# Optimization experiments

Hardware: AMD Instinct MI355X
Metric: run time of the kernel (lower is better)

The kernel has to match this reference:

```python
import jax, jax.numpy as jnp
import numpy as np

B, S, IN_F, OUT_F, GROUP = 2, 1024, 4096, 4096, 128
N_GROUPS = IN_F // GROUP  # 32


def setup_inputs() -> dict:
    key = jax.random.key(0)
    k1, k2, k3, k4 = jax.random.split(key, 4)
    x = jax.random.normal(k1, (B, S, IN_F), dtype=jnp.float32)
    # int4-range weights stored in int8, symmetric quant in [-7, 7]
    w_q = jax.random.randint(k2, (OUT_F, N_GROUPS, GROUP), -7, 8, dtype=jnp.int8)
    # per-(group, out_feature) scales, positive
    s_w = jax.random.uniform(k3, (N_GROUPS, OUT_F), dtype=jnp.float32,
                             minval=1e-3, maxval=2e-2)
    bias = jax.random.normal(k4, (OUT_F,), dtype=jnp.float32)
    return {"x": x, "w_q": w_q, "s_w": s_w, "bias": bias}


def reference(x, w_q, s_w, bias):
    # Faithful to QuantLinearW4Grouped.forward:
    #   y_g = einsum('ngk,ogk->ngo', x_f, w_f); y = (y_g * s_w[None]).sum(1) + bias
    # Expressed as a single fused einsum (identical math, no (n,g,o) intermediate).
    prefix = x.shape[:-1]
    orig_dtype = x.dtype
    xg = x.reshape(-1, N_GROUPS, GROUP).astype(jnp.float32)  # (n, g, k)
    w_f = w_q.astype(jnp.float32)                            # (o, g, k)
    y = jnp.einsum('ngk,ogk,go->no', xg, w_f, s_w)           # (n, o)
    y = y + bias.astype(y.dtype)
    return y.reshape(*prefix, OUT_F).astype(orig_dtype)
```

## Files before the change

### kernel.cpp

```cpp
#include <hip/hip_runtime.h>
#include <hip/hip_bf16.h>
#include <stdint.h>

#define M_TOK 2048
#define N_OUT 4096
#define K_IN  4096
#define GROUPSZ 128
#define NGRP  32

typedef signed char i8;
typedef int    intx4  __attribute__((ext_vector_type(4)));
typedef float  floatx4 __attribute__((ext_vector_type(4)));

#define XQ_BLOCKS (M_TOK)
#define WQ_BLOCKS (N_OUT * K_IN / 16 / 256)

__global__ __launch_bounds__(256) void quant_kernel(
    const float* __restrict__ x, const int* __restrict__ wq,
    i8* __restrict__ xq, i8* __restrict__ wq8, float* __restrict__ sx) {
  __shared__ float red[4];
  int b = blockIdx.x;
  int tid = threadIdx.x;
  if (b < XQ_BLOCKS) {
    const float* xr = x + (size_t)b * K_IN;
    int e0 = tid * 16;
    float4 v0 = *(const float4*)(xr + e0);
    float4 v1 = *(const float4*)(xr + e0 + 4);
    float4 v2 = *(const float4*)(xr + e0 + 8);
    float4 v3 = *(const float4*)(xr + e0 + 12);
    float m = fabsf(v0.x);
    m = fmaxf(m, fabsf(v0.y)); m = fmaxf(m, fabsf(v0.z)); m = fmaxf(m, fabsf(v0.w));
    m = fmaxf(m, fabsf(v1.x)); m = fmaxf(m, fabsf(v1.y)); m = fmaxf(m, fabsf(v1.z)); m = fmaxf(m, fabsf(v1.w));
    m = fmaxf(m, fabsf(v2.x)); m = fmaxf(m, fabsf(v2.y)); m = fmaxf(m, fabsf(v2.z)); m = fmaxf(m, fabsf(v2.w));
    m = fmaxf(m, fabsf(v3.x)); m = fmaxf(m, fabsf(v3.y)); m = fmaxf(m, fabsf(v3.z)); m = fmaxf(m, fabsf(v3.w));
#pragma unroll
    for (int off = 32; off > 0; off >>= 1)
      m = fmaxf(m, __shfl_xor(m, off, 64));
    int lane = tid & 63, wv = tid >> 6;
    if (lane == 0) red[wv] = m;
    __syncthreads();
    m = fmaxf(fmaxf(red[0], red[1]), fmaxf(red[2], red[3]));
    float inv = (m > 0.f) ? 127.f / m : 0.f;
    union { i8 q[16]; int4 v; } u;
    u.q[0]  = (i8)(int)rintf(v0.x * inv); u.q[1]  = (i8)(int)rintf(v0.y * inv);
    u.q[2]  = (i8)(int)rintf(v0.z * inv); u.q[3]  = (i8)(int)rintf(v0.w * inv);
    u.q[4]  = (i8)(int)rintf(v1.x * inv); u.q[5]  = (i8)(int)rintf(v1.y * inv);
    u.q[6]  = (i8)(int)rintf(v1.z * inv); u.q[7]  = (i8)(int)rintf(v1.w * inv);
    u.q[8]  = (i8)(int)rintf(v2.x * inv); u.q[9]  = (i8)(int)rintf(v2.y * inv);
    u.q[10] = (i8)(int)rintf(v2.z * inv); u.q[11] = (i8)(int)rintf(v2.w * inv);
    u.q[12] = (i8)(int)rintf(v3.x * inv); u.q[13] = (i8)(int)rintf(v3.y * inv);
    u.q[14] = (i8)(int)rintf(v3.z * inv); u.q[15] = (i8)(int)rintf(v3.w * inv);
    *(int4*)(xq + (size_t)b * K_IN + e0) = u.v;
    if (tid == 0) sx[b] = m * (1.f / 127.f);
  } else {
    size_t t = (size_t)(b - XQ_BLOCKS) * 256 + tid;
    size_t base = t * 16;
    const int* src = wq + base;
    int4 a0 = *(const int4*)(src);
    int4 a1 = *(const int4*)(src + 4);
    int4 a2 = *(const int4*)(src + 8);
    int4 a3 = *(const int4*)(src + 12);
    union { i8 q[16]; int4 v; } u;
    u.q[0]  = (i8)a0.x; u.q[1]  = (i8)a0.y; u.q[2]  = (i8)a0.z; u.q[3]  = (i8)a0.w;
    u.q[4]  = (i8)a1.x; u.q[5]  = (i8)a1.y; u.q[6]  = (i8)a1.z; u.q[7]  = (i8)a1.w;
    u.q[8]  = (i8)a2.x; u.q[9]  = (i8)a2.y; u.q[10] = (i8)a2.z; u.q[11] = (i8)a2.w;
    u.q[12] = (i8)a3.x; u.q[13] = (i8)a3.y; u.q[14] = (i8)a3.z; u.q[15] = (i8)a3.w;
    *(int4*)(wq8 + base) = u.v;
  }
}

#define BM 128
#define BN 128
#define BK 128

__global__ __launch_bounds__(512) void gemm_i8_kernel(
    const i8* __restrict__ Aq, const i8* __restrict__ Bq,
    const float* __restrict__ sx, const float* __restrict__ sw,
    const float* __restrict__ bias, float* __restrict__ C) {
  __shared__ i8 As[BM * BK];
  __shared__ i8 Bs[BN * BK];
  __shared__ float sws[NGRP * BN];
  __shared__ float sxs[BM];

  const int tid  = threadIdx.x;
  const int lane = tid & 63;
  const int wave = tid >> 6;
  const int bm = blockIdx.y;
  const int bn = blockIdx.x;
  const int wm = wave >> 1;
  const int wn = wave & 1;

  const int rowA0 = bm * BM;
  const int rowB0 = bn * BN;

  {
    int g = tid >> 4, c0 = (tid & 15) * 8;
    const float* src = sw + (size_t)g * N_OUT + rowB0 + c0;
    *(float4*)(sws + g * BN + c0)     = *(const float4*)(src);
    *(float4*)(sws + g * BN + c0 + 4) = *(const float4*)(src + 4);
    if (tid < BM) sxs[tid] = sx[rowA0 + tid];
  }

  floatx4 master[2][4];
#pragma unroll
  for (int i = 0; i < 2; ++i)
#pragma unroll
    for (int j = 0; j < 4; ++j) master[i][j] = (floatx4)0.0f;

  const int quad = lane >> 4;
  const int l16  = lane & 15;

  for (int k0 = 0, g = 0; k0 < K_IN; k0 += BK, ++g) {
    __syncthreads();
#pragma unroll
    for (int i = 0; i < 2; ++i) {
      int chunk = i * 512 + tid;
      int row = chunk >> 3;
      int csw = (chunk & 7) ^ (row & 7);
      int col = csw << 4;
      const i8* srcA = Aq + (size_t)(rowA0 + row) * K_IN + k0 + col;
      const i8* srcB = Bq + (size_t)(rowB0 + row) * K_IN + k0 + col;
      __builtin_amdgcn_global_load_lds(
          (const __attribute__((address_space(1))) void*)srcA,
          (__attribute__((address_space(3))) void*)(As + (size_t)(i * 512 + wave * 64) * 16),
          16, 0, 0);
      __builtin_amdgcn_global_load_lds(
          (const __attribute__((address_space(1))) void*)srcB,
          (__attribute__((address_space(3))) void*)(Bs + (size_t)(i * 512 + wave * 64) * 16),
          16, 0, 0);
    }
    __syncthreads();

    intx4 acci[2][4];
#pragma unroll
    for (int s = 0; s < 2; ++s) {
      const int kc = s * 4 + quad;
      intx4 av[2], bv[4];
#pragma unroll
      for (int i = 0; i < 2; ++i) {
        int r = wm * 32 + i * 16 + l16;
        av[i] = *(const intx4*)(As + (size_t)(r * 8 + (kc ^ (r & 7))) * 16);
      }
#pragma unroll
      for (int j = 0; j < 4; ++j) {
        int r = wn * 64 + j * 16 + l16;
        bv[j] = *(const intx4*)(Bs + (size_t)(r * 8 + (kc ^ (r & 7))) * 16);
      }
#pragma unroll
      for (int i = 0; i < 2; ++i)
#pragma unroll
        for (int j = 0; j < 4; ++j) {
          intx4 c0 = (s == 0) ? (intx4)0 : acci[i][j];
          acci[i][j] = __builtin_amdgcn_mfma_i32_16x16x64_i8(av[i], bv[j], c0, 0, 0, 0);
        }
    }

    float swv[4];
#pragma unroll
    for (int j = 0; j < 4; ++j)
      swv[j] = sws[g * BN + wn * 64 + j * 16 + l16];
#pragma unroll
    for (int i = 0; i < 2; ++i)
#pragma unroll
      for (int j = 0; j < 4; ++j)
#pragma unroll
        for (int r = 0; r < 4; ++r)
          master[i][j][r] += (float)acci[i][j][r] * swv[j];
  }

#pragma unroll
  for (int j = 0; j < 4; ++j) {
    int col = rowB0 + wn * 64 + j * 16 + l16;
    float bv = bias[col];
#pragma unroll
    for (int i = 0; i < 2; ++i) {
      int rloc = wm * 32 + i * 16 + quad * 4;
#pragma unroll
      for (int r = 0; r < 4; ++r) {
        C[(size_t)(rowA0 + rloc + r) * N_OUT + col] =
            master[i][j][r] * sxs[rloc + r] + bv;
      }
    }
  }
}

extern "C" void kernel_launch(void* const* d_in, const int* in_sizes, int n_in,
                              void* d_out, int out_size, void* d_ws, size_t ws_size,
                              hipStream_t stream) {
  const float* x    = (const float*)d_in[0];
  const int*   wq   = (const int*)d_in[1];
  const float* sw   = (const float*)d_in[2];
  const float* bias = (const float*)d_in[3];
  float* out = (float*)d_out;

  i8*    xq  = (i8*)d_ws;
  i8*    wq8 = (i8*)((char*)d_ws + (size_t)M_TOK * K_IN);
  float* sx  = (float*)((char*)d_ws + (size_t)M_TOK * K_IN
                                     + (size_t)N_OUT * K_IN);

  {
    int nblocks = XQ_BLOCKS + WQ_BLOCKS;
    quant_kernel<<<nblocks, 256, 0, stream>>>(x, wq, xq, wq8, sx);
  }
  {
    dim3 grid(N_OUT / BN, M_TOK / BM);
    gemm_i8_kernel<<<grid, 512, 0, stream>>>(xq, wq8, sx, sw, bias, out);
  }
}
```

Baseline: 171.7 us.

## Use 4-wave 64x64 warp tiles with magic-number int-to-float conversion

Halves the threads per GEMM block from 512 to 256, so each wave computes a 64x64 output tile (4x4 MFMA tiles) instead of 32x64. This raises register reuse of the A fragments and reduces LDS reads per MFMA. It also precomputes the global load addresses outside the K loop and seeds each MFMA accumulator with the 0x4B400000 bias. That lets the int32 result be turned into a float with a bitcast and a subtraction rather than a cvt instruction. The costs are higher register pressure from 64 float accumulators per lane, and the magic-number trick relies on group partial sums staying within the 2^22 range.

```diff
diff --git a/kernel.cpp b/kernel.cpp
--- a/kernel.cpp
+++ b/kernel.cpp
@@ -73,7 +73,7 @@
 #define BN 128
 #define BK 128
 
-__global__ __launch_bounds__(512) void gemm_i8_kernel(
+__global__ __launch_bounds__(256, 2) void gemm_i8_kernel(
     const i8* __restrict__ Aq, const i8* __restrict__ Bq,
     const float* __restrict__ sx, const float* __restrict__ sw,
     const float* __restrict__ bias, float* __restrict__ C) {
@@ -94,78 +94,84 @@
   const int rowB0 = bn * BN;
 
   {
-    int g = tid >> 4, c0 = (tid & 15) * 8;
+    int g = tid >> 3, c0 = (tid & 7) * 16;
     const float* src = sw + (size_t)g * N_OUT + rowB0 + c0;
-    *(float4*)(sws + g * BN + c0)     = *(const float4*)(src);
-    *(float4*)(sws + g * BN + c0 + 4) = *(const float4*)(src + 4);
+    float* dst = sws + g * BN + c0;
+    *(float4*)(dst)      = *(const float4*)(src);
+    *(float4*)(dst + 4)  = *(const float4*)(src + 4);
+    *(float4*)(dst + 8)  = *(const float4*)(src + 8);
+    *(float4*)(dst + 12) = *(const float4*)(src + 12);
     if (tid < BM) sxs[tid] = sx[rowA0 + tid];
   }
 
-  floatx4 master[2][4];
-#pragma unroll
-  for (int i = 0; i < 2; ++i)
+  const i8* srcA[4]; const i8* srcB[4];
+#pragma unroll
+  for (int i = 0; i < 4; ++i) {
+    int chunk = i * 256 + tid;
+    int row = chunk >> 3;
+    int col = ((chunk & 7) ^ (row & 7)) << 4;
+    srcA[i] = Aq + (size_t)(rowA0 + row) * K_IN + col;
+    srcB[i] = Bq + (size_t)(rowB0 + row) * K_IN + col;
+  }
+
+  floatx4 master[4][4];
+#pragma unroll
+  for (int i = 0; i < 4; ++i)
 #pragma unroll
     for (int j = 0; j < 4; ++j) master[i][j] = (floatx4)0.0f;
 
   const int quad = lane >> 4;
   const int l16  = lane & 15;
+  const int h    = l16 & 7;
+  const int x0   = (quad ^ h) * 16;
+  const int x1   = x0 ^ 64;
+
+  const intx4 MAGICV = {0x4B400000, 0x4B400000, 0x4B400000, 0x4B400000};
+  const float MAGICF = 12582912.0f;
 
   for (int k0 = 0, g = 0; k0 < K_IN; k0 += BK, ++g) {
     __syncthreads();
 #pragma unroll
-    for (int i = 0; i < 2; ++i) {
-      int chunk = i * 512 + tid;
-      int row = chunk >> 3;
-      int csw = (chunk & 7) ^ (row & 7);
-      int col = csw << 4;
-      const i8* srcA = Aq + (size_t)(rowA0 + row) * K_IN + k0 + col;
-      const i8* srcB = Bq + (size_t)(rowB0 + row) * K_IN + k0 + col;
+    for (int i = 0; i < 4; ++i) {
       __builtin_amdgcn_global_load_lds(
-          (const __attribute__((address_space(1))) void*)srcA,
-          (__attribute__((address_space(3))) void*)(As + (size_t)(i * 512 + wave * 64) * 16),
+          (const __attribute__((address_space(1))) void*)(srcA[i] + k0),
+          (__attribute__((address_space(3))) void*)(As + (size_t)(i * 256 + wave * 64) * 16),
           16, 0, 0);
       __builtin_amdgcn_global_load_lds(
-          (const __attribute__((address_space(1))) void*)srcB,
-          (__attribute__((address_space(3))) void*)(Bs + (size_t)(i * 512 + wave * 64) * 16),
+          (const __attribute__((address_space(1))) void*)(srcB[i] + k0),
+          (__attribute__((address_space(3))) void*)(Bs + (size_t)(i * 256 + wave * 64) * 16),
           16, 0, 0);
     }
     __syncthreads();
-
-    intx4 acci[2][4];
-#pragma unroll
-    for (int s = 0; s < 2; ++s) {
-      const int kc = s * 4 + quad;
-      intx4 av[2], bv[4];
-#pragma unroll
-      for (int i = 0; i < 2; ++i) {
-        int r = wm * 32 + i * 16 + l16;
-        av[i] = *(const intx4*)(As + (size_t)(r * 8 + (kc ^ (r & 7))) * 16);
-      }
-#pragma unroll
-      for (int j = 0; j < 4; ++j) {
-        int r = wn * 64 + j * 16 + l16;
-        bv[j] = *(const intx4*)(Bs + (size_t)(r * 8 + (kc ^ (r & 7))) * 16);
-      }
-#pragma unroll
-      for (int i = 0; i < 2; ++i)
-#pragma unroll
-        for (int j = 0; j < 4; ++j) {
-          intx4 c0 = (s == 0) ? (intx4)0 : acci[i][j];
-          acci[i][j] = __builtin_amdgcn_mfma_i32_16x16x64_i8(av[i], bv[j], c0, 0, 0, 0);
-        }
-    }
 
     float swv[4];
 #pragma unroll
     for (int j = 0; j < 4; ++j)
       swv[j] = sws[g * BN + wn * 64 + j * 16 + l16];
-#pragma unroll
-    for (int i = 0; i < 2; ++i)
-#pragma unroll
-      for (int j = 0; j < 4; ++j)
-#pragma unroll
-        for (int r = 0; r < 4; ++r)
-          master[i][j][r] += (float)acci[i][j][r] * swv[j];
+
+    intx4 a0[4], a1[4], b0[4], b1[4];
+#pragma unroll
+    for (int i = 0; i < 4; ++i) {
+      const i8* pa = As + (size_t)(wm * 64 + i * 16 + l16) * BK;
+      a0[i] = *(const intx4*)(pa + x0);
+      a1[i] = *(const intx4*)(pa + x1);
+    }
+#pragma unroll
+    for (int j = 0; j < 4; ++j) {
+      const i8* pb = Bs + (size_t)(wn * 64 + j * 16 + l16) * BK;
+      b0[j] = *(const intx4*)(pb + x0);
+      b1[j] = *(const intx4*)(pb + x1);
+    }
+
+#pragma unroll
+    for (int i = 0; i < 4; ++i)
+#pragma unroll
+      for (int j = 0; j < 4; ++j) {
+        intx4 acc = __builtin_amdgcn_mfma_i32_16x16x64_i8(a0[i], b0[j], MAGICV, 0, 0, 0);
+        acc = __builtin_amdgcn_mfma_i32_16x16x64_i8(a1[i], b1[j], acc, 0, 0, 0);
+        floatx4 t = __builtin_bit_cast(floatx4, acc) - MAGICF;
+        master[i][j] += t * swv[j];
+      }
   }
 
 #pragma unroll
@@ -173,8 +179,8 @@
     int col = rowB0 + wn * 64 + j * 16 + l16;
     float bv = bias[col];
 #pragma unroll
-    for (int i = 0; i < 2; ++i) {
-      int rloc = wm * 32 + i * 16 + quad * 4;
+    for (int i = 0; i < 4; ++i) {
+      int rloc = wm * 64 + i * 16 + quad * 4;
 #pragma unroll
       for (int r = 0; r < 4; ++r) {
         C[(size_t)(rowA0 + rloc + r) * N_OUT + col] =
@@ -204,6 +210,6 @@
   }
   {
     dim3 grid(N_OUT / BN, M_TOK / BM);
-    gemm_i8_kernel<<<grid, 512, 0, stream>>>(xq, wq8, sx, sw, bias, out);
+    gemm_i8_kernel<<<grid, 256, 0, stream>>>(xq, wq8, sx, sw, bias, out);
   }
 }
```

Result: no change. 173.3 us (+0.9%).
